# Kernel tuning notes

Hardware: AMD Instinct MI355X
Metric: run time of the kernel (lower is better)

Reference implementation:

```python
import jax, jax.numpy as jnp
import numpy as np

DIM = 1024
HEADS = 16
HEAD_DIM = DIM // HEADS
SCALE = HEAD_DIM ** -0.5
KSIZES = (1, 3, 5)


def setup_inputs() -> dict:
    key = jax.random.key(0)
    ks = jax.random.split(key, 16)
    b, n = 2, 2048
    s = 0.02
    inp = {
        "x": jax.random.normal(ks[0], (b, n, DIM), jnp.float32),
        "Wq": jax.random.normal(ks[1], (DIM, DIM), jnp.float32) * s,
        "Wk": jax.random.normal(ks[2], (DIM, DIM), jnp.float32) * s,
        "Wv": jax.random.normal(ks[3], (DIM, DIM), jnp.float32) * s,
        "Wo": jax.random.normal(ks[4], (DIM, DIM), jnp.float32) * s,
        "bo": jnp.zeros((DIM,), jnp.float32),
        "temperature": jnp.ones((1, HEADS, 1, 1), jnp.float32),
        "head_weights": jnp.ones((1, HEADS, 1, 1), jnp.float32),
    }
    # grouped Conv1d kernels: (out_ch=DIM, in_ch_per_group=DIM//HEADS, k)
    for i, k in enumerate(KSIZES):
        inp[f"conv_w{k}"] = jax.random.normal(ks[5 + i], (DIM, DIM // HEADS, k), jnp.float32) * s
        inp[f"conv_b{k}"] = jnp.zeros((DIM,), jnp.float32)
    return inp


def _grouped_conv1d(x_bdn, w, b, k):
    # x_bdn: [b, dim, n]; w: [dim, dim//HEADS, k]; 'same' padding for odd k
    y = jax.lax.conv_general_dilated(
        x_bdn, w, window_strides=(1,), padding=[(k // 2, k // 2)],
        dimension_numbers=("NCH", "OIH", "NCH"), feature_group_count=HEADS)
    return y + b[None, :, None]


def reference(x, Wq, Wk, Wv, Wo, bo, temperature, head_weights,
              conv_w1, conv_b1, conv_w3, conv_b3, conv_w5, conv_b5):
    b, n, _ = x.shape
    split = lambda t: t.reshape(b, n, HEADS, HEAD_DIM).transpose(0, 2, 1, 3)  # b h n d
    q = split(x @ Wq.T)
    k = split(x @ Wk.T)
    v = split(x @ Wv.T)
    dots = jnp.einsum("bhnd,bhmd->bhnm", q, k) * SCALE * temperature
    attn = jax.nn.softmax(dots, axis=-1)
    attn = attn * jax.nn.softmax(head_weights, axis=1)
    out = jnp.einsum("bhnm,bhmd->bhnd", attn, v)
    out = out.transpose(0, 2, 1, 3).reshape(b, n, DIM)  # b n (h d)
    oc = out.transpose(0, 2, 1)  # b dim n
    conv_sum = (_grouped_conv1d(oc, conv_w1, conv_b1, 1)
                + _grouped_conv1d(oc, conv_w3, conv_b3, 3)
                + _grouped_conv1d(oc, conv_w5, conv_b5, 5))
    n_scales = float(len(KSIZES))
    out_combined = out + conv_sum.transpose(0, 2, 1) / n_scales
    return out_combined @ Wo.T + bo
```

## Files before the change

kernel.cpp:

```cpp
#include <hip/hip_runtime.h>

#define DIM 1024
#define HEADS 16
#define HD 64
#define BATCH 2
#define SEQ 2048
#define MROWS (BATCH * SEQ)

typedef short s16x8 __attribute__((ext_vector_type(8)));
typedef short s16x4 __attribute__((ext_vector_type(4)));
typedef float f32x4 __attribute__((ext_vector_type(4)));

__device__ __forceinline__ short f2bf(float f) {
  unsigned u = __builtin_bit_cast(unsigned, f);
  u = u + 0x7fffu + ((u >> 16) & 1u);
  return (short)(u >> 16);
}

__device__ __forceinline__ float bf2f(short s) {
  unsigned u = ((unsigned)(unsigned short)s) << 16;
  return __builtin_bit_cast(float, u);
}

__device__ __forceinline__ float fexp2(float x) { return __builtin_amdgcn_exp2f(x); }

__device__ __forceinline__ unsigned cvtpk(float lo, float hi) {
  unsigned r;
  asm("v_cvt_pk_bf16_f32 %0, %1, %2" : "=v"(r) : "v"(lo), "v"(hi));
  return r;
}

__device__ __forceinline__ void gload16(const void* g, void* l) {
  __builtin_amdgcn_global_load_lds((__attribute__((address_space(1))) void*)g,
                                   (__attribute__((address_space(3))) void*)l,
                                   16, 0, 0);
}

__global__ __launch_bounds__(256)
void prep_all(const float* __restrict__ x, const float* __restrict__ Wq,
              const float* __restrict__ Wk, const float* __restrict__ Wv,
              const float* __restrict__ Wo, const float* __restrict__ w1,
              const float* __restrict__ b1, const float* __restrict__ w3,
              const float* __restrict__ b3, const float* __restrict__ w5,
              const float* __restrict__ b5, const float* __restrict__ temp,
              short* __restrict__ xb, short* __restrict__ wqb, short* __restrict__ wkb,
              short* __restrict__ wvb, short* __restrict__ wob, short* __restrict__ weff,
              float* __restrict__ bsum, float* __restrict__ scq) {
  const int blk = blockIdx.x;
  if (blk < 4096) {
    int i = blk * 256 + threadIdx.x;
    f32x4 v = *(const f32x4*)(x + (size_t)i * 4);
    s16x4 o;
#pragma unroll
    for (int j = 0; j < 4; ++j) o[j] = f2bf(v[j]);
    *(s16x4*)(xb + (size_t)i * 4) = o;
  } else if (blk < 8192) {
    int rel = blk - 4096;
    int w = rel >> 10;
    const float* in = (w == 0) ? Wq : (w == 1) ? Wk : (w == 2) ? Wv : Wo;
    short* out = (w == 0) ? wqb : (w == 1) ? wkb : (w == 2) ? wvb : wob;
    int i = (rel & 1023) * 256 + threadIdx.x;
    f32x4 v = *(const f32x4*)(in + (size_t)i * 4);
    s16x4 o;
#pragma unroll
    for (int j = 0; j < 4; ++j) o[j] = f2bf(v[j]);
    *(s16x4*)(out + (size_t)i * 4) = o;
  } else {
    int idx = (blk - 8192) * 256 + threadIdx.x;
    float t0 = w5[(size_t)idx * 5 + 0];
    float t1 = w5[(size_t)idx * 5 + 1] + w3[(size_t)idx * 3 + 0];
    float t2 = w5[(size_t)idx * 5 + 2] + w3[(size_t)idx * 3 + 1] + w1[idx];
    float t3 = w5[(size_t)idx * 5 + 3] + w3[(size_t)idx * 3 + 2];
    float t4 = w5[(size_t)idx * 5 + 4];
    weff[0 * DIM * 64 + idx] = f2bf(t0);
    weff[1 * DIM * 64 + idx] = f2bf(t1);
    weff[2 * DIM * 64 + idx] = f2bf(t2);
    weff[3 * DIM * 64 + idx] = f2bf(t3);
    weff[4 * DIM * 64 + idx] = f2bf(t4);
    if ((idx & 63) == 0) {
      int o = idx >> 6;
      bsum[o] = b1[o] + b3[o] + b5[o];
    }
    if (idx < HEADS) scq[idx] = 0.125f * temp[idx] * 1.44269504f;
  }
}

#define QSTAGE(BUF, KT)                                                                \
  _Pragma("unroll") for (int i = 0; i < 2; ++i) {                                      \
    int cbase = i * 512 + wave * 64;                                                   \
    int c = cbase + lane;                                                              \
    int row = c >> 3;                                                                  \
    int cb = ((c ^ row) & 7) << 4;                                                     \
    gload16((const char*)A + ((size_t)(brow + row) * DIM + (KT)) * 2 + cb,             \
            (char*)&As[BUF][0][0] + cbase * 16);                                       \
    gload16((const char*)Bq + ((size_t)(bcol + row) * DIM + (KT)) * 2 + cb,            \
            (char*)&Bs[BUF][0][0][0] + cbase * 16);                                    \
    gload16((const char*)Bk + ((size_t)(bcol + row) * DIM + (KT)) * 2 + cb,            \
            (char*)&Bs[BUF][1][0][0] + cbase * 16);                                    \
    gload16((const char*)Bv + ((size_t)(bcol + row) * DIM + (KT)) * 2 + cb,            \
            (char*)&Bs[BUF][2][0][0] + cbase * 16);                                    \
  }

__global__ __launch_bounds__(512)
void qkv_fused(const short* __restrict__ A, const short* __restrict__ Bq,
               const short* __restrict__ Bk, const short* __restrict__ Bv,
               const float* __restrict__ scq, short* __restrict__ oq,
               short* __restrict__ ok, short* __restrict__ ov) {
  __shared__ __align__(16) short As[2][128][64];
  __shared__ __align__(16) short Bs[2][3][128][64];
  const int tid = threadIdx.x;
  const int lane = tid & 63, wave = tid >> 6;
  const int fr = lane & 15, fg = lane >> 4;
  const int wr = wave >> 1, wc = wave & 1;
  const int brow = blockIdx.y * 128, bcol = blockIdx.x * 128;

  int offA[2][2], offB[2][4];
#pragma unroll
  for (int kk = 0; kk < 2; ++kk) {
    int sw = ((kk * 4 + fg) ^ (fr & 7)) << 4;
#pragma unroll
    for (int m = 0; m < 2; ++m) offA[kk][m] = (wr * 32 + m * 16 + fr) * 128 + sw;
#pragma unroll
    for (int n = 0; n < 4; ++n) offB[kk][n] = (wc * 64 + n * 16 + fr) * 128 + sw;
  }

  f32x4 acc[3][2][4] = {};

  QSTAGE(0, 0);
  __syncthreads();

  for (int kt = 0; kt < DIM; kt += 64) {
    const int cur = (kt >> 6) & 1;
    if (kt + 64 < DIM) { QSTAGE(cur ^ 1, kt + 64); }
    const char* Ab = (const char*)&As[cur][0][0];
    const char* Bb = (const char*)&Bs[cur][0][0][0];
#pragma unroll
    for (int kk = 0; kk < 2; ++kk) {
      s16x8 af[2];
#pragma unroll
      for (int m = 0; m < 2; ++m) af[m] = *(const s16x8*)(Ab + offA[kk][m]);
#pragma unroll
      for (int z = 0; z < 3; ++z) {
        s16x8 bfr[4];
#pragma unroll
        for (int n = 0; n < 4; ++n) bfr[n] = *(const s16x8*)(Bb + z * 16384 + offB[kk][n]);
#pragma unroll
        for (int m = 0; m < 2; ++m)
#pragma unroll
          for (int n = 0; n < 4; ++n)
            acc[z][m][n] =
                __builtin_amdgcn_mfma_f32_16x16x32_bf16(af[m], bfr[n], acc[z][m][n], 0, 0, 0);
      }
    }
    __syncthreads();
  }

  const int hh = (bcol >> 6) + wc;
  const float sv = scq[hh];
#pragma unroll
  for (int m = 0; m < 2; ++m) {
#pragma unroll
    for (int n = 0; n < 4; ++n) {
      int i0 = brow + wr * 32 + m * 16 + fg * 4;
      int dd = n * 16 + fr;
#pragma unroll
      for (int r = 0; r < 4; ++r) {
        int i = i0 + r;
        size_t qko = (((size_t)(i >> 11) * HEADS + hh) * SEQ + (i & (SEQ - 1))) * HD + dd;
        oq[qko] = f2bf(acc[0][m][n][r] * sv);
        ok[qko] = f2bf(acc[1][m][n][r]);
      }
      s16x4 o4;
#pragma unroll
      for (int r = 0; r < 4; ++r) o4[r] = f2bf(acc[2][m][n][r]);
      *(s16x4*)&ov[(((size_t)(i0 >> 11) * HEADS + hh) * HD + dd) * SEQ + (i0 & (SEQ - 1))] = o4;
    }
  }
}

#define OSTAGE(BUF, KT)                                                              \
  _Pragma("unroll") for (int i = 0; i < 2; ++i) {                                    \
    int cbase = i * 512 + wave * 64;                                                 \
    int c = cbase + lane;                                                            \
    int row = c >> 3;                                                                \
    int cb = ((c ^ row) & 7) << 4;                                                   \
    gload16((const char*)A + ((size_t)(brow + row) * DIM + (KT)) * 2 + cb,           \
            (char*)&As[BUF][0][0] + cbase * 16);                                     \
    gload16((const char*)Bw + ((size_t)(bcol + row) * DIM + (KT)) * 2 + cb,          \
            (char*)&Bs[BUF][0][0] + cbase * 16);                                     \
  }

__global__ __launch_bounds__(512)
void out_gemm(const short* __restrict__ A, const short* __restrict__ Bw,
              const float* __restrict__ bias, float* __restrict__ out) {
  __shared__ __align__(16) short As[2][128][64];
  __shared__ __align__(16) short Bs[2][128][64];
  const int tid = threadIdx.x;
  const int lane = tid & 63, wave = tid >> 6;
  const int fr = lane & 15, fg = lane >> 4;
  const int wr = wave >> 1, wc = wave & 1;
  const int brow = blockIdx.y * 128, bcol = blockIdx.x * 128;
  f32x4 acc[2][4] = {};

  int offA[2][2], offB[2][4];
#pragma unroll
  for (int kk = 0; kk < 2; ++kk) {
    int sw = ((kk * 4 + fg) ^ (fr & 7)) << 4;
#pragma unroll
    for (int m = 0; m < 2; ++m) offA[kk][m] = (wr * 32 + m * 16 + fr) * 128 + sw;
#pragma unroll
    for (int n = 0; n < 4; ++n) offB[kk][n] = (wc * 64 + n * 16 + fr) * 128 + sw;
  }

  OSTAGE(0, 0);
  __syncthreads();

  for (int kt = 0; kt < DIM; kt += 64) {
    const int cur = (kt >> 6) & 1;
    if (kt + 64 < DIM) { OSTAGE(cur ^ 1, kt + 64); }
    const char* Ab = (const char*)&As[cur][0][0];
    const char* Bb = (const char*)&Bs[cur][0][0];
#pragma unroll
    for (int kk = 0; kk < 2; ++kk) {
      s16x8 af[2], bfr[4];
#pragma unroll
      for (int m = 0; m < 2; ++m) af[m] = *(const s16x8*)(Ab + offA[kk][m]);
#pragma unroll
      for (int n = 0; n < 4; ++n) bfr[n] = *(const s16x8*)(Bb + offB[kk][n]);
#pragma unroll
      for (int m = 0; m < 2; ++m)
#pragma unroll
        for (int n = 0; n < 4; ++n)
          acc[m][n] = __builtin_amdgcn_mfma_f32_16x16x32_bf16(af[m], bfr[n], acc[m][n], 0, 0, 0);
    }
    __syncthreads();
  }

#pragma unroll
  for (int m = 0; m < 2; ++m) {
#pragma unroll
    for (int n = 0; n < 4; ++n) {
      int i0 = brow + wr * 32 + m * 16 + fg * 4;
      int j = bcol + wc * 64 + n * 16 + fr;
#pragma unroll
      for (int r = 0; r < 4; ++r)
        out[(size_t)(i0 + r) * DIM + j] = acc[m][n][r] + bias[j];
    }
  }
}

#define STAGE(BUF, KT)                                                                   \
  gload16((const char*)K + (bhoff + (size_t)((KT) + srow) * HD) * 2 + scs,               \
          (char*)&Ks[BUF][0][0] + wbyte);                                                \
  gload16((const char*)Vt + (vbase + (size_t)srow * SEQ + (KT)) * 2 + scs,               \
          (char*)&Vs[BUF][0][0] + wbyte);

#define ATTN_TILE(CUR, STG, KTSTG, DOSTAGE, WAITSTR)                                     \
  {                                                                                      \
    asm volatile("s_waitcnt " WAITSTR ::: "memory");                                     \
    __builtin_amdgcn_s_barrier();                                                        \
    asm volatile("" ::: "memory");                                                       \
    if (DOSTAGE) { STAGE(STG, KTSTG); }                                                  \
    f32x4 st[4] = {};                                                                    \
    __builtin_amdgcn_s_setprio(1);                                                       \
    _Pragma("unroll") for (int ks = 0; ks < 2; ++ks) {                                   \
      _Pragma("unroll") for (int kf = 0; kf < 4; ++kf) {                                 \
        const s16x8 kfr = *(const s16x8*)((const char*)&Ks[CUR][0][0] + off[ks][kf]);    \
        st[kf] = __builtin_amdgcn_mfma_f32_16x16x32_bf16(kfr, qf_[ks], st[kf], 0, 0, 0); \
      }                                                                                  \
    }                                                                                    \
    __builtin_amdgcn_s_setprio(0);                                                       \
    float rsum = 0.f;                                                                    \
    _Pragma("unroll") for (int kf = 0; kf < 4; ++kf) {                                   \
      float p0 = fexp2(st[kf][0]), p1 = fexp2(st[kf][1]);                                \
      float p2 = fexp2(st[kf][2]), p3 = fexp2(st[kf][3]);                                \
      rsum += (p0 + p1) + (p2 + p3);                                                     \
      uint2 pk;                                                                          \
      pk.x = cvtpk(p0, p1);                                                              \
      pk.y = cvtpk(p2, p3);                                                              \
      *(uint2*)((char*)Psb + pwoff[kf]) = pk;                                            \
    }                                                                                    \
    lrow += rsum;                                                                        \
    __builtin_amdgcn_s_setprio(1);                                                       \
    _Pragma("unroll") for (int ks2 = 0; ks2 < 2; ++ks2) {                                \
      const s16x8 pfr = *(const s16x8*)((const char*)Psb + proff[ks2]);                  \
      _Pragma("unroll") for (int vf = 0; vf < 4; ++vf) {                                 \
        const s16x8 vfr = *(const s16x8*)((const char*)&Vs[CUR][0][0] + off[ks2][vf]);   \
        oacc[vf] = __builtin_amdgcn_mfma_f32_16x16x32_bf16(vfr, pfr, oacc[vf], 0, 0, 0); \
      }                                                                                  \
    }                                                                                    \
    __builtin_amdgcn_s_setprio(0);                                                       \
  }

__global__ __launch_bounds__(512)
void attn_fwd(const short* __restrict__ Q, const short* __restrict__ K,
              const short* __restrict__ Vt, short* __restrict__ att,
              const float* __restrict__ hw) {
  __shared__ __align__(16) short Ks[3][64][64];
  __shared__ __align__(16) short Vs[3][64][64];
  __shared__ __align__(16) short Ps[8][16][72];
  const int bid = blockIdx.x;
  const int bh = (bid & 7) * 4 + (bid >> 7);
  const int h = bh & (HEADS - 1);
  const int qbase = ((bid >> 3) & 15) * 128;
  const int tid = threadIdx.x;
  const int lane = tid & 63, wave = tid >> 6;
  const int fr = lane & 15, fg = lane >> 4;
  const int frx = (fr & 7);

  float hmax = -1e30f;
  for (int i = 0; i < HEADS; ++i) hmax = fmaxf(hmax, hw[i]);
  float hsum = 0.f;
  for (int i = 0; i < HEADS; ++i) hsum += expf(hw[i] - hmax);
  const float hwsm = expf(hw[h] - hmax) / hsum;

  const size_t bhoff = (size_t)bh * SEQ * HD;
  const int qrow = qbase + wave * 16 + fr;
  s16x8 qf_[2];
#pragma unroll
  for (int ks = 0; ks < 2; ++ks)
    qf_[ks] = *(const s16x8*)&Q[bhoff + (size_t)qrow * HD + ks * 32 + fg * 8];

  int off[2][4];
#pragma unroll
  for (int ks = 0; ks < 2; ++ks)
#pragma unroll
    for (int f = 0; f < 4; ++f)
      off[ks][f] = (f * 16 + fr) * 128 + (((ks * 4 + fg) ^ frx) << 4);
  int pwoff[4], proff[2];
#pragma unroll
  for (int kf = 0; kf < 4; ++kf) pwoff[kf] = ((wave * 16 + fr) * 72 + kf * 16 + fg * 4) * 2;
#pragma unroll
  for (int ks2 = 0; ks2 < 2; ++ks2) proff[ks2] = ((wave * 16 + fr) * 72 + ks2 * 32 + fg * 8) * 2;
  const char* Psb = (const char*)&Ps[0][0][0];

  f32x4 oacc[4] = {};
  float lrow = 0.f;

  const int srow = tid >> 3;
  const int scs = ((tid & 7) ^ (srow & 7)) << 4;
  const int wbyte = wave * 64 * 16;
  const size_t vbase = (size_t)bh * HD * SEQ;

  STAGE(0, 0);
  STAGE(1, 64);

  for (int ktg = 0; ktg + 192 <= SEQ; ktg += 192) {
    ATTN_TILE(0, 2, ktg + 128, true, "vmcnt(2)");
    ATTN_TILE(1, 0, ktg + 192, true, "vmcnt(2)");
    ATTN_TILE(2, 1, ktg + 256, true, "vmcnt(2)");
  }
  ATTN_TILE(0, 0, 0, false, "vmcnt(2)");
  ATTN_TILE(1, 0, 0, false, "vmcnt(0)");

  lrow += __shfl_xor(lrow, 16);
  lrow += __shfl_xor(lrow, 32);

  const int b = bh >> 4;
  const float isc = hwsm / lrow;
#pragma unroll
  for (int vf = 0; vf < 4; ++vf) {
    s16x4 o4;
#pragma unroll
    for (int r = 0; r < 4; ++r) o4[r] = f2bf(oacc[vf][r] * isc);
    *(s16x4*)&att[((size_t)b * SEQ + qrow) * DIM + h * HD + vf * 16 + fg * 4] = o4;
  }
}

#define CP 68
__global__ __launch_bounds__(256)
void conv_mfma(const short* __restrict__ attb, const short* __restrict__ weff,
               const float* __restrict__ bsum, short* __restrict__ comb) {
  __shared__ __align__(16) short As[132][CP];
  __shared__ __align__(16) short Ws[5][64][CP];
  const int b = blockIdx.z, g = blockIdx.y, n0 = blockIdx.x * 128;
  const int tid = threadIdx.x, lane = tid & 63, wave = tid >> 6;
  const int fr = lane & 15, fg = lane >> 4;

  const short* abase = attb + (size_t)b * SEQ * DIM + g * 64;
  for (int idx = tid; idx < 132 * 8; idx += 256) {
    int r = idx >> 3, cb = (idx & 7) * 8;
    int rn = n0 + r - 2;
    s16x8 v = {};
    if (rn >= 0 && rn < SEQ) v = *(const s16x8*)&abase[(size_t)rn * DIM + cb];
    *(s16x8*)&As[r][cb] = v;
  }
  for (int idx = tid; idx < 5 * 64 * 8; idx += 256) {
    int t = idx >> 9;
    int rem = idx & 511;
    int o = rem >> 3, cb = (rem & 7) * 8;
    s16x8 v = *(const s16x8*)&weff[((size_t)t * DIM + g * 64 + o) * 64 + cb];
    *(s16x8*)&Ws[t][o][cb] = v;
  }
  __syncthreads();

  f32x4 acc[2][4] = {};
#pragma unroll
  for (int dt = 0; dt < 5; ++dt) {
#pragma unroll
    for (int kk = 0; kk < 2; ++kk) {
      const int ko = kk * 32 + fg * 8;
      s16x8 af[2], bfr[4];
#pragma unroll
      for (int m = 0; m < 2; ++m)
        af[m] = *(const s16x8*)&As[wave * 32 + m * 16 + fr + dt][ko];
#pragma unroll
      for (int n = 0; n < 4; ++n) bfr[n] = *(const s16x8*)&Ws[dt][n * 16 + fr][ko];
#pragma unroll
      for (int m = 0; m < 2; ++m)
#pragma unroll
        for (int n = 0; n < 4; ++n)
          acc[m][n] = __builtin_amdgcn_mfma_f32_16x16x32_bf16(af[m], bfr[n], acc[m][n], 0, 0, 0);
    }
  }

#pragma unroll
  for (int m = 0; m < 2; ++m) {
#pragma unroll
    for (int n = 0; n < 4; ++n) {
      int lrow0 = wave * 32 + m * 16 + fg * 4;
      int col = n * 16 + fr;
      float bs = bsum[g * 64 + col];
#pragma unroll
      for (int r = 0; r < 4; ++r) {
        int lr = lrow0 + r;
        float res = bf2f(As[lr + 2][col]);
        float outv = res + (acc[m][n][r] + bs) * (1.f / 3.f);
        comb[((size_t)b * SEQ + n0 + lr) * DIM + g * 64 + col] = f2bf(outv);
      }
    }
  }
}

extern "C" void kernel_launch(void* const* d_in, const int* in_sizes, int n_in, void* d_out,
                              int out_size, void* d_ws, size_t ws_size, hipStream_t stream) {
  const float* x = (const float*)d_in[0];
  const float* Wq = (const float*)d_in[1];
  const float* Wk = (const float*)d_in[2];
  const float* Wv = (const float*)d_in[3];
  const float* Wo = (const float*)d_in[4];
  const float* bo = (const float*)d_in[5];
  const float* temp = (const float*)d_in[6];
  const float* hw = (const float*)d_in[7];
  const float* w1 = (const float*)d_in[8];
  const float* b1 = (const float*)d_in[9];
  const float* w3 = (const float*)d_in[10];
  const float* b3 = (const float*)d_in[11];
  const float* w5 = (const float*)d_in[12];
  const float* b5 = (const float*)d_in[13];

  char* ws = (char*)d_ws;
  const size_t MB = 1u << 20;
  short* xb = (short*)(ws);
  short* wqb = (short*)(ws + 8 * MB);
  short* wkb = (short*)(ws + 10 * MB);
  short* wvb = (short*)(ws + 12 * MB);
  short* wob = (short*)(ws + 14 * MB);
  short* qb = (short*)(ws + 16 * MB);
  short* kb = (short*)(ws + 24 * MB);
  short* vtb = (short*)(ws + 32 * MB);
  short* attb = (short*)(ws + 40 * MB);
  short* comb = (short*)(ws + 48 * MB);
  short* weff = (short*)(ws + 56 * MB);
  float* bsum = (float*)(ws + 57 * MB);
  float* scq = (float*)(ws + 57 * MB + 4096);

  prep_all<<<8448, 256, 0, stream>>>(x, Wq, Wk, Wv, Wo, w1, b1, w3, b3, w5, b5, temp, xb, wqb,
                                     wkb, wvb, wob, weff, bsum, scq);

  qkv_fused<<<dim3(DIM / 128, MROWS / 128), 512, 0, stream>>>(xb, wqb, wkb, wvb, scq, qb, kb, vtb);

  attn_fwd<<<512, 512, 0, stream>>>(qb, kb, vtb, attb, hw);

  conv_mfma<<<dim3(SEQ / 128, HEADS, BATCH), 256, 0, stream>>>(attb, weff, bsum, comb);

  dim3 go(DIM / 128, MROWS / 128);
  out_gemm<<<go, 512, 0, stream>>>(comb, wob, bo, (float*)d_out);
}
```

Baseline: 116.8 us.

## Load V fragments directly from global into registers instead of LDS staging

V tiles are no longer staged through shared memory. Each wave now reads its V MFMA operands straight from global memory into registers at the start of every key tile, and only K stays in the triple-buffered LDS pipeline, with the wait counts relaxed to match. This saves LDS space, LDS writes and reads, and one async load per stage. In exchange all eight waves fetch the same V tile redundantly from L2. Because the V loads are issued after the K prefetch and global loads complete in order, waiting on V may also wait on the K prefetch, and the V latency is exposed within each tile.

```diff
diff --git a/kernel.cpp b/kernel.cpp
--- a/kernel.cpp
+++ b/kernel.cpp
@@ -251,16 +251,18 @@
 
 #define STAGE(BUF, KT)                                                                   \
   gload16((const char*)K + (bhoff + (size_t)((KT) + srow) * HD) * 2 + scs,               \
-          (char*)&Ks[BUF][0][0] + wbyte);                                                \
-  gload16((const char*)Vt + (vbase + (size_t)srow * SEQ + (KT)) * 2 + scs,               \
-          (char*)&Vs[BUF][0][0] + wbyte);
-
-#define ATTN_TILE(CUR, STG, KTSTG, DOSTAGE, WAITSTR)                                     \
+          (char*)&Ks[BUF][0][0] + wbyte);
+
+#define ATTN_TILE(CUR, STG, KTSTG, KTCUR, DOSTAGE, WAITSTR)                              \
   {                                                                                      \
     asm volatile("s_waitcnt " WAITSTR ::: "memory");                                     \
     __builtin_amdgcn_s_barrier();                                                        \
     asm volatile("" ::: "memory");                                                       \
     if (DOSTAGE) { STAGE(STG, KTSTG); }                                                  \
+    s16x8 vfr[2][4];                                                                     \
+    _Pragma("unroll") for (int ks2 = 0; ks2 < 2; ++ks2)                                  \
+      _Pragma("unroll") for (int vf = 0; vf < 4; ++vf)                                   \
+        vfr[ks2][vf] = *(const s16x8*)&Vt[vroff[vf] + (KTCUR) + ks2 * 32];               \
     f32x4 st[4] = {};                                                                    \
     __builtin_amdgcn_s_setprio(1);                                                       \
     _Pragma("unroll") for (int ks = 0; ks < 2; ++ks) {                                   \
@@ -285,8 +287,8 @@
     _Pragma("unroll") for (int ks2 = 0; ks2 < 2; ++ks2) {                                \
       const s16x8 pfr = *(const s16x8*)((const char*)Psb + proff[ks2]);                  \
       _Pragma("unroll") for (int vf = 0; vf < 4; ++vf) {                                 \
-        const s16x8 vfr = *(const s16x8*)((const char*)&Vs[CUR][0][0] + off[ks2][vf]);   \
-        oacc[vf] = __builtin_amdgcn_mfma_f32_16x16x32_bf16(vfr, pfr, oacc[vf], 0, 0, 0); \
+        oacc[vf] =                                                                       \
+            __builtin_amdgcn_mfma_f32_16x16x32_bf16(vfr[ks2][vf], pfr, oacc[vf], 0, 0, 0); \
       }                                                                                  \
     }                                                                                    \
     __builtin_amdgcn_s_setprio(0);                                                       \
@@ -297,7 +299,6 @@
               const short* __restrict__ Vt, short* __restrict__ att,
               const float* __restrict__ hw) {
   __shared__ __align__(16) short Ks[3][64][64];
-  __shared__ __align__(16) short Vs[3][64][64];
   __shared__ __align__(16) short Ps[8][16][72];
   const int bid = blockIdx.x;
   const int bh = (bid & 7) * 4 + (bid >> 7);
@@ -334,24 +335,28 @@
   for (int ks2 = 0; ks2 < 2; ++ks2) proff[ks2] = ((wave * 16 + fr) * 72 + ks2 * 32 + fg * 8) * 2;
   const char* Psb = (const char*)&Ps[0][0][0];
 
+  int vroff[4];
+#pragma unroll
+  for (int vf = 0; vf < 4; ++vf)
+    vroff[vf] = (int)((unsigned)bh * HD * SEQ) + (vf * 16 + fr) * SEQ + fg * 8;
+
   f32x4 oacc[4] = {};
   float lrow = 0.f;
 
   const int srow = tid >> 3;
   const int scs = ((tid & 7) ^ (srow & 7)) << 4;
   const int wbyte = wave * 64 * 16;
-  const size_t vbase = (size_t)bh * HD * SEQ;
 
   STAGE(0, 0);
   STAGE(1, 64);
 
   for (int ktg = 0; ktg + 192 <= SEQ; ktg += 192) {
-    ATTN_TILE(0, 2, ktg + 128, true, "vmcnt(2)");
-    ATTN_TILE(1, 0, ktg + 192, true, "vmcnt(2)");
-    ATTN_TILE(2, 1, ktg + 256, true, "vmcnt(2)");
-  }
-  ATTN_TILE(0, 0, 0, false, "vmcnt(2)");
-  ATTN_TILE(1, 0, 0, false, "vmcnt(0)");
+    ATTN_TILE(0, 2, ktg + 128, ktg, true, "vmcnt(1)");
+    ATTN_TILE(1, 0, ktg + 192, ktg + 64, true, "vmcnt(1)");
+    ATTN_TILE(2, 1, ktg + 256, ktg + 128, true, "vmcnt(1)");
+  }
+  ATTN_TILE(0, 0, 0, 1920, false, "vmcnt(1)");
+  ATTN_TILE(1, 0, 0, 1984, false, "vmcnt(0)");
 
   lrow += __shfl_xor(lrow, 16);
   lrow += __shfl_xor(lrow, 32);
```

Result: slower. 225.0 us (+92.6%).

## Triple-buffer output GEMM with vmcnt waits and one barrier per tile

Applied to the files above, without the earlier changes.

Moves the output projection GEMM from a double-buffered LDS loop with two __syncthreads per K-tile to a three-buffer pipeline that keeps two tiles in flight. Each tile now waits only for its own global-to-LDS loads via s_waitcnt vmcnt, then takes a single barrier. The aim is to hide global load latency better and cut synchronisation stalls. In exchange it uses 50% more LDS, which may lower occupancy, and the fully unrolled schedule depends on correct vmcnt accounting.

```diff
diff --git a/kernel.cpp b/kernel.cpp
--- a/kernel.cpp
+++ b/kernel.cpp
@@ -190,11 +190,32 @@
             (char*)&Bs[BUF][0][0] + cbase * 16);                                     \
   }
 
+#define OTILE(CUR, STG, KTSTG, DOSTG, WAITSTR)                                       \
+  {                                                                                  \
+    asm volatile("s_waitcnt " WAITSTR ::: "memory");                                 \
+    __builtin_amdgcn_s_barrier();                                                    \
+    asm volatile("" ::: "memory");                                                   \
+    if (DOSTG) { OSTAGE(STG, KTSTG); }                                               \
+    const char* Ab = (const char*)&As[CUR][0][0];                                    \
+    const char* Bb = (const char*)&Bs[CUR][0][0];                                    \
+    _Pragma("unroll") for (int kk = 0; kk < 2; ++kk) {                               \
+      s16x8 af[2], bfr[4];                                                           \
+      _Pragma("unroll") for (int m = 0; m < 2; ++m)                                  \
+        af[m] = *(const s16x8*)(Ab + offA[kk][m]);                                   \
+      _Pragma("unroll") for (int n = 0; n < 4; ++n)                                  \
+        bfr[n] = *(const s16x8*)(Bb + offB[kk][n]);                                  \
+      _Pragma("unroll") for (int m = 0; m < 2; ++m)                                  \
+        _Pragma("unroll") for (int n = 0; n < 4; ++n)                                \
+          acc[m][n] =                                                                \
+              __builtin_amdgcn_mfma_f32_16x16x32_bf16(af[m], bfr[n], acc[m][n], 0, 0, 0); \
+    }                                                                                \
+  }
+
 __global__ __launch_bounds__(512)
 void out_gemm(const short* __restrict__ A, const short* __restrict__ Bw,
               const float* __restrict__ bias, float* __restrict__ out) {
-  __shared__ __align__(16) short As[2][128][64];
-  __shared__ __align__(16) short Bs[2][128][64];
+  __shared__ __align__(16) short As[3][128][64];
+  __shared__ __align__(16) short Bs[3][128][64];
   const int tid = threadIdx.x;
   const int lane = tid & 63, wave = tid >> 6;
   const int fr = lane & 15, fg = lane >> 4;
@@ -213,28 +234,18 @@
   }
 
   OSTAGE(0, 0);
-  __syncthreads();
-
-  for (int kt = 0; kt < DIM; kt += 64) {
-    const int cur = (kt >> 6) & 1;
-    if (kt + 64 < DIM) { OSTAGE(cur ^ 1, kt + 64); }
-    const char* Ab = (const char*)&As[cur][0][0];
-    const char* Bb = (const char*)&Bs[cur][0][0];
-#pragma unroll
-    for (int kk = 0; kk < 2; ++kk) {
-      s16x8 af[2], bfr[4];
-#pragma unroll
-      for (int m = 0; m < 2; ++m) af[m] = *(const s16x8*)(Ab + offA[kk][m]);
-#pragma unroll
-      for (int n = 0; n < 4; ++n) bfr[n] = *(const s16x8*)(Bb + offB[kk][n]);
-#pragma unroll
-      for (int m = 0; m < 2; ++m)
-#pragma unroll
-        for (int n = 0; n < 4; ++n)
-          acc[m][n] = __builtin_amdgcn_mfma_f32_16x16x32_bf16(af[m], bfr[n], acc[m][n], 0, 0, 0);
-    }
-    __syncthreads();
-  }
+  OSTAGE(1, 64);
+
+  for (int g = 0; g < 4; ++g) {
+    const int kt = g * 192;
+    OTILE(0, 2, kt + 128, true, "vmcnt(4)");
+    OTILE(1, 0, kt + 192, true, "vmcnt(4)");
+    OTILE(2, 1, kt + 256, true, "vmcnt(4)");
+  }
+  OTILE(0, 2, 896, true, "vmcnt(4)");
+  OTILE(1, 0, 960, true, "vmcnt(4)");
+  OTILE(2, 0, 0, false, "vmcnt(4)");
+  OTILE(0, 0, 0, false, "vmcnt(0)");
 
 #pragma unroll
   for (int m = 0; m < 2; ++m) {
```

After: 114.5 us. About the same (-2.0%).
